# Performance work log

Measured on AMD Instinct MI355X. Metric: run time of the kernel, lower is better.

## Reference

```python
import jax, jax.numpy as jnp
import numpy as np

N = 50000      # nodes
E = 1_600_000  # edges (avg degree 32)
G = 2000       # graphs in batch
H = 2          # attention heads
C = 64         # out_channels
IN = 64        # in_channels
NEG_SLOPE = 0.2


def setup_inputs() -> dict:
    key = jax.random.key(0)
    ks = jax.random.split(key, 6)
    x = jax.random.normal(ks[0], (N, IN), dtype=jnp.float32)
    edge_index = jax.random.randint(ks[1], (2, E), 0, N, dtype=jnp.int32)
    batch = jnp.sort(jax.random.randint(ks[2], (N,), 0, G, dtype=jnp.int32))
    # GATConv params: lin weight [H*C, IN] (glorot-ish), att vectors, bias [C]
    W = jax.random.normal(ks[3], (H * C, IN), dtype=jnp.float32) * (1.0 / np.sqrt(IN))
    att_src = jax.random.normal(ks[4], (1, H, C), dtype=jnp.float32) * 0.1
    att_dst = jax.random.normal(ks[5], (1, H, C), dtype=jnp.float32) * 0.1
    bias = jnp.zeros((C,), dtype=jnp.float32)
    return {"x": x, "edge_index": edge_index, "batch": batch,
            "W": W, "att_src": att_src, "att_dst": att_dst, "bias": bias}


def reference(x, edge_index, batch, W, att_src, att_dst, bias):
    # --- GATConv (PyG semantics: add_self_loops=True, concat=False -> head mean + bias) ---
    loops = jnp.arange(N, dtype=edge_index.dtype)
    src = jnp.concatenate([edge_index[0], loops])  # [E+N]
    dst = jnp.concatenate([edge_index[1], loops])  # [E+N]

    xp = (x @ W.T).reshape(N, H, C)                 # projected node feats [N,H,C]
    a_src = jnp.sum(xp * att_src, axis=-1)          # [N,H]
    a_dst = jnp.sum(xp * att_dst, axis=-1)          # [N,H]

    e = jax.nn.leaky_relu(a_src[src] + a_dst[dst], NEG_SLOPE)  # [E+N,H]
    # segment softmax over incoming edges of each destination node
    m = jax.ops.segment_max(e, dst, num_segments=N)            # [N,H]
    e = jnp.exp(e - m[dst])
    s = jax.ops.segment_sum(e, dst, num_segments=N)            # [N,H]
    alpha = e / s[dst]                                         # [E+N,H]

    msg = xp[src] * alpha[:, :, None]                          # [E+N,H,C]
    out = jax.ops.segment_sum(msg, dst, num_segments=N)        # [N,H,C]
    h_nodes = out.mean(axis=1) + bias                          # [N,C]

    # --- global_mean_pool ---
    sums = jax.ops.segment_sum(h_nodes, batch, num_segments=G)                     # [G,C]
    cnt = jax.ops.segment_sum(jnp.ones((N, 1), h_nodes.dtype), batch, num_segments=G)
    h_graphs = sums / jnp.maximum(cnt, 1.0)                                        # [G,C]
    return (h_nodes, h_graphs)
```

## Files before the change

### kernel.cpp

```cpp
#include <hip/hip_runtime.h>
#include <hip/hip_bf16.h>

#define H 2
#define C 64
#define IN_CH 64
#define HC (H*C)
#define NEG_SLOPE 0.2f
#define NBUCK_MAX 1024
#define SBLK 512
#define PBLK 2048
#define BKT 64
#define CAP 3072

__global__ __launch_bounds__(128) void fused_kernel(
    const float* __restrict__ x, const float* __restrict__ W,
    const float* __restrict__ att_src, const float* __restrict__ att_dst,
    const int* __restrict__ batch, const int* __restrict__ edge,
    __hip_bfloat16* __restrict__ xp, float* __restrict__ asrc,
    float* __restrict__ adst, int* __restrict__ cnt, int* __restrict__ staged,
    int* __restrict__ gbeg, int N, int E, int G, int nbuck) {
    const int t = threadIdx.x;
    if (blockIdx.x < SBLK) {
        const int bid = blockIdx.x;
        const int chunkE = (E + SBLK - 1) / SBLK;
        const int* srcE = edge;
        const int* dstE = edge + E;
        __shared__ int lh[NBUCK_MAX], bse[NBUCK_MAX], lcur[NBUCK_MAX];
        for (int i = t; i < nbuck; i += 128) { lh[i] = 0; lcur[i] = 0; }
        __syncthreads();
        int beg = bid * chunkE, end = min(beg + chunkE, E);
        for (int i = beg + t; i < end; i += 128)
            atomicAdd(&lh[dstE[i] >> 6], 1);
        __syncthreads();
        for (int i = t; i < nbuck; i += 128)
            bse[i] = atomicAdd(&cnt[i], lh[i]);
        __syncthreads();
        for (int i = beg + t; i < end; i += 128) {
            int s = srcE[i], d = dstE[i];
            int b = d >> 6;
            int l = atomicAdd(&lcur[b], 1);
            staged[(size_t)b * CAP + bse[b] + l] = s | ((d & 63) << 20);
        }
        return;
    }
    int pb = blockIdx.x - SBLK;
    {
        int i = pb * 128 + t;
        if (i < N) {
            int bi = batch[i];
            if (i == 0) {
                for (int g = 0; g <= bi; g++) gbeg[g] = 0;
            } else {
                int bp = batch[i - 1];
                for (int g = bp + 1; g <= bi; g++) gbeg[g] = i;
            }
            if (i == N - 1)
                for (int g = bi + 1; g <= G; g++) gbeg[g] = N;
        }
    }
    float w[64];
    const float4* wr = reinterpret_cast<const float4*>(W + (size_t)t * IN_CH);
#pragma unroll
    for (int q = 0; q < 16; q++) {
        float4 v = wr[q];
        w[4 * q] = v.x; w[4 * q + 1] = v.y; w[4 * q + 2] = v.z; w[4 * q + 3] = v.w;
    }
    float a_s = att_src[t], a_d = att_dst[t];
    int lane = t & 63, head = t >> 6;
    for (int n = pb; n < N; n += PBLK) {
        const float* xr = x + (size_t)n * IN_CH;
        float acc = 0.f;
#pragma unroll
        for (int k = 0; k < 64; k++) acc = fmaf(w[k], xr[k], acc);
        xp[(size_t)n * HC + t] = __float2bfloat16(acc);
        float as = acc * a_s, ad = acc * a_d;
#pragma unroll
        for (int d = 32; d > 0; d >>= 1) {
            as += __shfl_xor(as, d, 64);
            ad += __shfl_xor(ad, d, 64);
        }
        if (lane == 0) {
            asrc[(size_t)n * H + head] = as;
            adst[(size_t)n * H + head] = ad;
        }
    }
}

template<int NB>
__device__ __forceinline__ void gfma(const char* __restrict__ xb,
                                     const int* __restrict__ si,
                                     const float* __restrict__ swl,
                                     uint laneoff, float& accx, float& accy) {
    uint bu[NB];
#pragma unroll
    for (int j = 0; j < NB; j++) {
        uint boff = (uint)si[j] + laneoff;
        bu[j] = *reinterpret_cast<const uint*>(xb + boff);
    }
#pragma unroll
    for (int j = 0; j < NB; j++) {
        float w = swl[2 * j];
        accx = fmaf(w, __uint_as_float(bu[j] << 16), accx);
        accy = fmaf(w, __uint_as_float(bu[j] & 0xffff0000u), accy);
    }
}

__global__ __launch_bounds__(256, 4) void csragg_kernel(
    const __hip_bfloat16* __restrict__ xp, const float* __restrict__ asrc,
    const float* __restrict__ adst, const int* __restrict__ cnt,
    const int* __restrict__ staged_all, const float* __restrict__ bias,
    float* __restrict__ out, int N) {
    __shared__ int lcsr[CAP];
    __shared__ int loff[BKT + 1];
    __shared__ int lh[BKT], cur[BKT];
    __shared__ int sidx[4][32];
    __shared__ float swf[4][64];
    int b = blockIdx.x, tid = threadIdx.x;
    int lane = tid & 63, wid = tid >> 6;
    int size = cnt[b];
    const int* st = staged_all + (size_t)b * CAP;
    if (tid < BKT) lh[tid] = 0;
    __syncthreads();
    for (int i = tid; i < size; i += 256)
        atomicAdd(&lh[st[i] >> 20], 1);
    __syncthreads();
    if (wid == 0) {
        int v = lh[lane];
        int inc = v;
#pragma unroll
        for (int d = 1; d < 64; d <<= 1) {
            int u = __shfl_up(inc, d, 64);
            if (lane >= d) inc += u;
        }
        loff[lane] = inc - v;
        cur[lane] = inc - v;
        if (lane == 63) loff[BKT] = inc;
    }
    __syncthreads();
    for (int i = tid; i < size; i += 256) {
        int e = st[i];
        int pos = atomicAdd(&cur[e >> 20], 1);
        lcsr[pos] = (e & 0xFFFFF) << 8;
    }
    __syncthreads();
    const uint* xpw = reinterpret_cast<const uint*>(xp);
    const char* xb = reinterpret_cast<const char*>(xp);
    int cl = lane & 31, hsel = lane >> 5;
    uint laneoff = (uint)lane * 4u;
    int* si = sidx[wid];
    float* swl = swf[wid] + hsel;
    for (int k = 0; k < 16; k++) {
        int nd = wid * 16 + k;
        int n = b * BKT + nd;
        if (n >= N) break;
        int o0 = loff[nd];
        int deg = loff[nd + 1] - o0;
        float adh = adst[2 * n + hsel];
        float es = asrc[2 * n + hsel] + adh;
        es = (es > 0.f) ? es : NEG_SLOPE * es;
        float wself = __expf(es);
        float ssum = (cl == 0) ? wself : 0.f;
        uint u = xpw[(size_t)n * 64 + lane];
        float accx = wself * __uint_as_float(u << 16);
        float accy = wself * __uint_as_float(u & 0xffff0000u);
        for (int base = 0; base < deg; base += 32) {
            int i = base + cl;
            int boff = 0;
            float w = 0.f;
            if (i < deg) {
                boff = lcsr[o0 + i];
                float t = asrc[(boff >> 7) + hsel] + adh;
                t = (t > 0.f) ? t : NEG_SLOPE * t;
                w = __expf(t);
            }
            ssum += w;
            if (!hsel) si[cl] = boff;
            swl[2 * cl] = w;
            int nb = min(deg - base, 32);
            if (nb > 16) gfma<32>(xb, si, swl, laneoff, accx, accy);
            else         gfma<16>(xb, si, swl, laneoff, accx, accy);
        }
#pragma unroll
        for (int d = 16; d > 0; d >>= 1) ssum += __shfl_xor(ssum, d, 64);
        float inv = 1.f / ssum;
        accx *= inv;
        accy *= inv;
        float ox = 0.5f * (accx + __shfl_xor(accx, 32, 64));
        float oy = 0.5f * (accy + __shfl_xor(accy, 32, 64));
        if (lane < 32) {
            float vx = ox + bias[2 * cl];
            float vy = oy + bias[2 * cl + 1];
            *reinterpret_cast<float2*>(out + (size_t)n * C + 2 * cl) =
                make_float2(vx, vy);
        }
    }
}

__global__ __launch_bounds__(256) void pool_kernel(const float* __restrict__ hn,
                                                   const int* __restrict__ gbeg,
                                                   float* __restrict__ outG, int G) {
    int g = blockIdx.x;
    int c = threadIdx.x & 63, r = threadIdx.x >> 6;
    int beg = gbeg[g], end = gbeg[g + 1];
    float s = 0.f;
    for (int n = beg + r; n < end; n += 4) s += hn[(size_t)n * C + c];
    __shared__ float red[256];
    red[threadIdx.x] = s;
    __syncthreads();
    if (r == 0) {
        float tot = red[c] + red[64 + c] + red[128 + c] + red[192 + c];
        outG[(size_t)g * C + c] = tot / fmaxf((float)(end - beg), 1.f);
    }
}

extern "C" void kernel_launch(void* const* d_in, const int* in_sizes, int n_in,
                              void* d_out, int out_size, void* d_ws, size_t ws_size,
                              hipStream_t stream) {
    const float* x       = (const float*)d_in[0];
    const int*   edge    = (const int*)d_in[1];
    const int*   batch   = (const int*)d_in[2];
    const float* W       = (const float*)d_in[3];
    const float* att_src = (const float*)d_in[4];
    const float* att_dst = (const float*)d_in[5];
    const float* bias    = (const float*)d_in[6];

    int N = in_sizes[0] / IN_CH;
    int E = in_sizes[1] / 2;
    int G = out_size / C - N;
    int nbuck = (N + BKT - 1) / BKT;

    char* p = (char*)d_ws;
    auto alloc = [&](size_t bytes) {
        char* r = p;
        p += (bytes + 255) & ~(size_t)255;
        return r;
    };
    __hip_bfloat16* xp = (__hip_bfloat16*)alloc((size_t)N * HC * 2);
    float* asrc    = (float*)alloc((size_t)N * H * 4);
    float* adst    = (float*)alloc((size_t)N * H * 4);
    int*   cnt     = (int*)alloc((size_t)nbuck * 4);
    int*   staged  = (int*)alloc((size_t)nbuck * CAP * 4);
    int*   gbeg    = (int*)alloc((size_t)(G + 1) * 4);

    hipMemsetAsync(cnt, 0, (size_t)nbuck * 4, stream);
    fused_kernel<<<SBLK + PBLK, 128, 0, stream>>>(x, W, att_src, att_dst, batch, edge,
                                                  xp, asrc, adst, cnt, staged, gbeg,
                                                  N, E, G, nbuck);
    csragg_kernel<<<nbuck, 256, 0, stream>>>(xp, asrc, adst, cnt, staged, bias,
                                             (float*)d_out, N);
    pool_kernel<<<G, 256, 0, stream>>>((const float*)d_out, gbeg,
                                       (float*)d_out + (size_t)N * C, G);
}
```

Before: 190.1 us.

## Split aggregation buckets into halves and fuse mean pooling via atomics

```diff
diff --git a/kernel.cpp b/kernel.cpp
--- a/kernel.cpp
+++ b/kernel.cpp
@@ -11,6 +11,7 @@
 #define PBLK 2048
 #define BKT 64
 #define CAP 3072
+#define LCAP 1536
 
 __global__ __launch_bounds__(128) void fused_kernel(
     const float* __restrict__ x, const float* __restrict__ W,
@@ -18,7 +19,8 @@
     const int* __restrict__ batch, const int* __restrict__ edge,
     __hip_bfloat16* __restrict__ xp, float* __restrict__ asrc,
     float* __restrict__ adst, int* __restrict__ cnt, int* __restrict__ staged,
-    int* __restrict__ gbeg, int N, int E, int G, int nbuck) {
+    int* __restrict__ gbeg, float* __restrict__ outG,
+    int N, int E, int G, int nbuck) {
     const int t = threadIdx.x;
     if (blockIdx.x < SBLK) {
         const int bid = blockIdx.x;
@@ -45,6 +47,10 @@
     }
     int pb = blockIdx.x - SBLK;
     {
+        int i2 = pb * 128 + t;
+        if (i2 < G * C) outG[i2] = 0.f;
+    }
+    {
         int i = pb * 128 + t;
         if (i < N) {
             int bi = batch[i];
@@ -105,42 +111,48 @@
     }
 }
 
-__global__ __launch_bounds__(256, 4) void csragg_kernel(
+__global__ __launch_bounds__(256, 6) void csragg_kernel(
     const __hip_bfloat16* __restrict__ xp, const float* __restrict__ asrc,
     const float* __restrict__ adst, const int* __restrict__ cnt,
     const int* __restrict__ staged_all, const float* __restrict__ bias,
-    float* __restrict__ out, int N) {
-    __shared__ int lcsr[CAP];
-    __shared__ int loff[BKT + 1];
-    __shared__ int lh[BKT], cur[BKT];
+    const int* __restrict__ batch, const int* __restrict__ gbeg,
+    float* __restrict__ out, float* __restrict__ outG, int N) {
+    __shared__ int lcsr[LCAP];
+    __shared__ int loff[33];
+    __shared__ int lh[32], cur[32];
     __shared__ int sidx[4][32];
     __shared__ float swf[4][64];
-    int b = blockIdx.x, tid = threadIdx.x;
+    int bid = blockIdx.x, tid = threadIdx.x;
+    int b = bid >> 1, half = bid & 1;
     int lane = tid & 63, wid = tid >> 6;
     int size = cnt[b];
     const int* st = staged_all + (size_t)b * CAP;
-    if (tid < BKT) lh[tid] = 0;
-    __syncthreads();
-    for (int i = tid; i < size; i += 256)
-        atomicAdd(&lh[st[i] >> 20], 1);
-    __syncthreads();
-    if (wid == 0) {
+    if (tid < 32) lh[tid] = 0;
+    __syncthreads();
+    for (int i = tid; i < size; i += 256) {
+        int e = st[i];
+        if (((e >> 25) & 1) == half) atomicAdd(&lh[(e >> 20) & 31], 1);
+    }
+    __syncthreads();
+    if (wid == 0 && lane < 32) {
         int v = lh[lane];
         int inc = v;
 #pragma unroll
-        for (int d = 1; d < 64; d <<= 1) {
+        for (int d = 1; d < 32; d <<= 1) {
             int u = __shfl_up(inc, d, 64);
             if (lane >= d) inc += u;
         }
         loff[lane] = inc - v;
         cur[lane] = inc - v;
-        if (lane == 63) loff[BKT] = inc;
+        if (lane == 31) loff[32] = inc;
     }
     __syncthreads();
     for (int i = tid; i < size; i += 256) {
         int e = st[i];
-        int pos = atomicAdd(&cur[e >> 20], 1);
-        lcsr[pos] = (e & 0xFFFFF) << 8;
+        if (((e >> 25) & 1) == half) {
+            int pos = atomicAdd(&cur[(e >> 20) & 31], 1);
+            lcsr[pos] = (e & 0xFFFFF) << 8;
+        }
     }
     __syncthreads();
     const uint* xpw = reinterpret_cast<const uint*>(xp);
@@ -149,9 +161,9 @@
     uint laneoff = (uint)lane * 4u;
     int* si = sidx[wid];
     float* swl = swf[wid] + hsel;
-    for (int k = 0; k < 16; k++) {
-        int nd = wid * 16 + k;
-        int n = b * BKT + nd;
+    for (int k = 0; k < 8; k++) {
+        int nd = wid * 8 + k;
+        int n = b * BKT + half * 32 + nd;
         if (n >= N) break;
         int o0 = loff[nd];
         int deg = loff[nd + 1] - o0;
@@ -192,24 +204,11 @@
             float vy = oy + bias[2 * cl + 1];
             *reinterpret_cast<float2*>(out + (size_t)n * C + 2 * cl) =
                 make_float2(vx, vy);
-        }
-    }
-}
-
-__global__ __launch_bounds__(256) void pool_kernel(const float* __restrict__ hn,
-                                                   const int* __restrict__ gbeg,
-                                                   float* __restrict__ outG, int G) {
-    int g = blockIdx.x;
-    int c = threadIdx.x & 63, r = threadIdx.x >> 6;
-    int beg = gbeg[g], end = gbeg[g + 1];
-    float s = 0.f;
-    for (int n = beg + r; n < end; n += 4) s += hn[(size_t)n * C + c];
-    __shared__ float red[256];
-    red[threadIdx.x] = s;
-    __syncthreads();
-    if (r == 0) {
-        float tot = red[c] + red[64 + c] + red[128 + c] + red[192 + c];
-        outG[(size_t)g * C + c] = tot / fmaxf((float)(end - beg), 1.f);
+            int g = batch[n];
+            float invc = 1.f / (float)(gbeg[g + 1] - gbeg[g]);
+            atomicAdd(&outG[(size_t)g * C + 2 * cl], vx * invc);
+            atomicAdd(&outG[(size_t)g * C + 2 * cl + 1], vy * invc);
+        }
     }
 }
 
@@ -241,13 +240,13 @@
     int*   cnt     = (int*)alloc((size_t)nbuck * 4);
     int*   staged  = (int*)alloc((size_t)nbuck * CAP * 4);
     int*   gbeg    = (int*)alloc((size_t)(G + 1) * 4);
+    float* out     = (float*)d_out;
+    float* outG    = out + (size_t)N * C;
 
     hipMemsetAsync(cnt, 0, (size_t)nbuck * 4, stream);
     fused_kernel<<<SBLK + PBLK, 128, 0, stream>>>(x, W, att_src, att_dst, batch, edge,
                                                   xp, asrc, adst, cnt, staged, gbeg,
-                                                  N, E, G, nbuck);
-    csragg_kernel<<<nbuck, 256, 0, stream>>>(xp, asrc, adst, cnt, staged, bias,
-                                             (float*)d_out, N);
-    pool_kernel<<<G, 256, 0, stream>>>((const float*)d_out, gbeg,
-                                       (float*)d_out + (size_t)N * C, G);
-}
+                                                  outG, N, E, G, nbuck);
+    csragg_kernel<<<nbuck * 2, 256, 0, stream>>>(xp, asrc, adst, cnt, staged, bias,
+                                                 batch, gbeg, out, outG, N);
+}
```

Result: slower. 215.7 us (+13.5%).
